# Performance work log

Hardware: AMD Instinct MI355X
Metric: run time of the kernel (lower is better)

The kernel has to match this reference:

```python
import jax, jax.numpy as jnp
import numpy as np

B, S, F = 4, 2048, 1024
D_K = 1024


def setup_inputs() -> dict:
    key = jax.random.key(0)
    ks = jax.random.split(key, 9)
    s_in = 1.0 / np.sqrt(F)
    s_dk = 1.0 / np.sqrt(D_K)
    return {
        "x": jax.random.normal(ks[0], (B, S, F), jnp.float32),
        "Wq": jax.random.normal(ks[1], (F, D_K), jnp.float32) * s_in,
        "bq": jax.random.normal(ks[2], (D_K,), jnp.float32) * s_in,
        "Wk": jax.random.normal(ks[3], (F, D_K), jnp.float32) * s_in,
        "bk": jax.random.normal(ks[4], (D_K,), jnp.float32) * s_in,
        "Wv": jax.random.normal(ks[5], (F, D_K), jnp.float32) * s_in,
        "bv": jax.random.normal(ks[6], (D_K,), jnp.float32) * s_in,
        "Wo": jax.random.normal(ks[7], (D_K, F), jnp.float32) * s_dk,
        "bo": jax.random.normal(ks[8], (F,), jnp.float32) * s_dk,
    }


def reference(x, Wq, bq, Wk, bk, Wv, bv, Wo, bo):
    d_k = Wq.shape[1]
    # init_keys(x): keys/values are projections of the same sequence
    keys = jnp.einsum("bsf,fd->bsd", x, Wk) + bk      # [B,S,d_k]
    values = jnp.einsum("bsf,fd->bsd", x, Wv) + bv    # [B,S,d_k]
    queries = jnp.einsum("bsf,fd->bsd", x, Wq) + bq   # [B,S,d_k]
    # scores[b, q, k] = <queries[b,q], keys[b,k]> / sqrt(d_k)
    scores = jnp.einsum("bqd,bkd->bqk", queries, keys) / jnp.sqrt(
        jnp.asarray(d_k, x.dtype)
    )
    # NOTE: original softmaxes over dim=-2, i.e. over the QUERY axis
    attn = jax.nn.softmax(scores, axis=-2)            # [B,Sq,Sk]
    ctx = jnp.einsum("bqk,bkd->bqd", attn, values)    # [B,S,d_k]
    out = jnp.einsum("bqd,df->bqf", ctx, Wo) + bo     # [B,S,F]
    return out
```

## Files before the change

kernel.cpp:

```cpp
#include <hip/hip_runtime.h>
#include <hip/hip_bf16.h>
#include <cstdint>

typedef __bf16 bf16_t;
typedef __bf16 bf16x8 __attribute__((ext_vector_type(8)));
typedef float  floatx4 __attribute__((ext_vector_type(4)));

typedef const __attribute__((address_space(1))) unsigned int* gptr_t;
typedef __attribute__((address_space(3))) unsigned int* lptr_t;

static __device__ __forceinline__ void gl2lds16(const bf16_t* g, bf16_t* l) {
  __builtin_amdgcn_global_load_lds((gptr_t)g, (lptr_t)l, 16, 0, 0);
}

template<int OUT_BF16, int HAS_BIAS, int EXP_COLSUM, int SPLIT3>
__global__ __launch_bounds__(256, 4)
void gemm_nt(const bf16_t* __restrict__ A, const bf16_t* __restrict__ Bt,
             void* __restrict__ Cv, const float* __restrict__ bias,
             float* __restrict__ L,
             int M, int N, int K, int ldC, float alpha,
             long sA, long sB, long sC,
             long co0, long co1, long co2)
{
  __shared__ __align__(16) bf16_t smem[2 * 128 * 32];
  bf16_t* As = smem;
  bf16_t* Bs = smem + 128 * 32;

  const int bz = blockIdx.z;
  A  += bz * sA;
  Bt += bz * sB;

  const int gn0 = blockIdx.x * 128;
  const int m0  = blockIdx.y * 128;
  const int tid  = threadIdx.x;
  const int lane = tid & 63;
  const int wave = tid >> 6;
  const int wm   = (wave >> 1) * 64;
  const int wn   = (wave & 1) * 64;
  const int lm   = lane & 15;
  const int quad = lane >> 4;

  int n0 = gn0;
  bf16_t* Cb = (bf16_t*)Cv;
  float*  Cf = (float*)Cv;
  if (SPLIT3) {
    const int which = gn0 >> 10;
    n0 = gn0 & 1023;
    Cb += (which == 0) ? co0 : (which == 1) ? co1 : co2;
  }

  const int srow   = lane >> 2;
  const int schunk = (lane & 3) * 8;

  floatx4 acc[4][4];
#pragma unroll
  for (int i = 0; i < 4; ++i)
#pragma unroll
    for (int j = 0; j < 4; ++j)
      acc[i][j] = (floatx4)(0.f);

  for (int kk = 0; kk < K; kk += 32) {
    __syncthreads();
#pragma unroll
    for (int t = 0; t < 2; ++t) {
      const int r = wave * 32 + t * 16 + srow;
      gl2lds16(A  + (long)(m0  + r) * K + kk + schunk, &As[r * 32 + schunk]);
      gl2lds16(Bt + (long)(gn0 + r) * K + kk + schunk, &Bs[r * 32 + schunk]);
    }
    __syncthreads();

    bf16x8 af[4], bfr[4];
#pragma unroll
    for (int i = 0; i < 4; ++i)
      af[i] = *(const bf16x8*)&As[(wm + i * 16 + lm) * 32 + quad * 8];
#pragma unroll
    for (int j = 0; j < 4; ++j)
      bfr[j] = *(const bf16x8*)&Bs[(wn + j * 16 + lm) * 32 + quad * 8];
#pragma unroll
    for (int i = 0; i < 4; ++i)
#pragma unroll
      for (int j = 0; j < 4; ++j)
        acc[i][j] = __builtin_amdgcn_mfma_f32_16x16x32_bf16(af[i], bfr[j],
                                                            acc[i][j], 0, 0, 0);
  }

  if (OUT_BF16) {
    __syncthreads();
    bf16_t* myEp = smem + wave * (16 * 68);
    const int r8 = lane >> 3;
    const int c8 = lane & 7;
    float cs[4] = {0.f, 0.f, 0.f, 0.f};
#pragma unroll
    for (int i = 0; i < 4; ++i) {
#pragma unroll
      for (int j = 0; j < 4; ++j) {
        const float bv = HAS_BIAS ? bias[gn0 + wn + j * 16 + lm] : 0.f;
#pragma unroll
        for (int r = 0; r < 4; ++r) {
          float v = alpha * acc[i][j][r];
          if (EXP_COLSUM) { v = __expf(v); cs[j] += v; }
          v += bv;
          myEp[(quad * 4 + r) * 68 + j * 16 + lm] = (bf16_t)v;
        }
      }
#pragma unroll
      for (int t = 0; t < 2; ++t) {
        const int row = t * 8 + r8;
        const bf16x8 vv = *(const bf16x8*)&myEp[row * 68 + c8 * 8];
        *(bf16x8*)&Cb[bz * sC + (long)(m0 + wm + i * 16 + row) * ldC
                      + n0 + wn + c8 * 8] = vv;
      }
    }
    if (EXP_COLSUM) {
#pragma unroll
      for (int j = 0; j < 4; ++j) {
        float v = cs[j];
        v += __shfl_xor(v, 16);
        v += __shfl_xor(v, 32);
        if (quad == 0)
          atomicAdd(&L[bz * N + gn0 + wn + j * 16 + lm], v);
      }
    }
  } else {
#pragma unroll
    for (int j = 0; j < 4; ++j) {
      const int cn = n0 + wn + j * 16 + lm;
      const float bv = HAS_BIAS ? bias[gn0 + wn + j * 16 + lm] : 0.f;
#pragma unroll
      for (int i = 0; i < 4; ++i) {
        const int rbase = m0 + wm + i * 16 + quad * 4;
#pragma unroll
        for (int r = 0; r < 4; ++r)
          Cf[bz * sC + (long)(rbase + r) * ldC + cn] = alpha * acc[i][j][r] + bv;
      }
    }
  }
}

template<typename TIN>
__global__ void transpose_to_bf16(const TIN* __restrict__ in, bf16_t* __restrict__ out,
                                  int rows, int cols, long sIn, long sOut)
{
  __shared__ float tile[32][33];
  const int bz = blockIdx.z;
  in  += bz * sIn;
  out += bz * sOut;
  const int c0 = blockIdx.x * 32;
  const int r0 = blockIdx.y * 32;
  const int tx = threadIdx.x;
  const int ty = threadIdx.y;
#pragma unroll
  for (int i = 0; i < 32; i += 8)
    tile[ty + i][tx] = (float)in[(long)(r0 + ty + i) * cols + (c0 + tx)];
  __syncthreads();
#pragma unroll
  for (int i = 0; i < 32; i += 8)
    out[(long)(c0 + ty + i) * rows + (r0 + tx)] = (bf16_t)tile[tx][ty + i];
}

__global__ void transpose3_to_bf16(const float* __restrict__ w0,
                                   const float* __restrict__ w1,
                                   const float* __restrict__ w2,
                                   bf16_t* __restrict__ out, int rows, int cols)
{
  __shared__ float tile[32][33];
  const int z = blockIdx.z;
  const float* in = (z == 0) ? w0 : (z == 1) ? w1 : w2;
  out += (long)z * rows * cols;
  const int c0 = blockIdx.x * 32;
  const int r0 = blockIdx.y * 32;
  const int tx = threadIdx.x;
  const int ty = threadIdx.y;
#pragma unroll
  for (int i = 0; i < 32; i += 8)
    tile[ty + i][tx] = in[(long)(r0 + ty + i) * cols + (c0 + tx)];
  __syncthreads();
#pragma unroll
  for (int i = 0; i < 32; i += 8)
    out[(long)(c0 + ty + i) * rows + (r0 + tx)] = (bf16_t)tile[tx][ty + i];
}

__global__ void cvt_f32_to_bf16(const float* __restrict__ in, bf16_t* __restrict__ out,
                                long n)
{
  const long i = ((long)blockIdx.x * blockDim.x + threadIdx.x) * 4;
  if (i >= n) return;
  const float4 v = *(const float4*)(in + i);
  struct alignas(8) B4 { bf16_t a, b, c, d; };
  B4 o; o.a = (bf16_t)v.x; o.b = (bf16_t)v.y; o.c = (bf16_t)v.z; o.d = (bf16_t)v.w;
  *(B4*)(out + i) = o;
}

__global__ void concat3(const float* __restrict__ a, const float* __restrict__ b,
                        const float* __restrict__ c, float* __restrict__ o)
{
  const int i = blockIdx.x * blockDim.x + threadIdx.x;
  const float* s = (i < 1024) ? a : (i < 2048) ? b : c;
  o[i] = s[i & 1023];
}

__global__ __launch_bounds__(256)
void scale_vt(bf16_t* __restrict__ Vt, const float* __restrict__ L, int S)
{
  const long base = ((long)blockIdx.x * blockDim.x + threadIdx.x) * 8;
  const int b  = (int)(base >> 21);
  const int s0 = (int)(base & (long)(S - 1));
  const float* Lb = L + b * S + s0;
  bf16x8 v = *(const bf16x8*)(Vt + base);
#pragma unroll
  for (int j = 0; j < 8; ++j)
    v[j] = (bf16_t)((float)v[j] / Lb[j]);
  *(bf16x8*)(Vt + base) = v;
}

extern "C" void kernel_launch(void* const* d_in, const int* in_sizes, int n_in,
                              void* d_out, int out_size, void* d_ws, size_t ws_size,
                              hipStream_t stream)
{
  const int Bz = 4, S = 2048, F = 1024, DK = 1024;
  const int M = Bz * S;

  const float* x  = (const float*)d_in[0];
  const float* Wq = (const float*)d_in[1];
  const float* bq = (const float*)d_in[2];
  const float* Wk = (const float*)d_in[3];
  const float* bk = (const float*)d_in[4];
  const float* Wv = (const float*)d_in[5];
  const float* bv = (const float*)d_in[6];
  const float* Wo = (const float*)d_in[7];
  const float* bo = (const float*)d_in[8];

  char* ws = (char*)d_ws;
  const size_t MB = 1ull << 20;
  bf16_t* Xb   = (bf16_t*)(ws + 0);
  bf16_t* V    = (bf16_t*)(ws + 16 * MB);
  bf16_t* Sc   = (bf16_t*)(ws + 0);
  bf16_t* Q    = (bf16_t*)(ws + 32 * MB);
  bf16_t* Ctx  = (bf16_t*)(ws + 32 * MB);
  bf16_t* Kb   = (bf16_t*)(ws + 48 * MB);
  bf16_t* Vt   = (bf16_t*)(ws + 64 * MB);
  float*  bcat = (float*)(ws + 64 * MB);
  bf16_t* WcatT= (bf16_t*)(ws + 80 * MB);
  float*  L    = (float*)(ws + 80 * MB);
  bf16_t* WoT  = (bf16_t*)(ws + 86 * MB);

  const long coQ = 16 * MB;
  const long coK = 24 * MB;
  const long coV =  8 * MB;

  cvt_f32_to_bf16<<<(M * F) / 1024, 256, 0, stream>>>(x, Xb, (long)M * F);

  dim3 tb(32, 8);
  transpose3_to_bf16<<<dim3(DK / 32, F / 32, 3), tb, 0, stream>>>(Wq, Wk, Wv, WcatT, F, DK);
  transpose_to_bf16<float><<<dim3(F / 32, DK / 32, 1), tb, 0, stream>>>(Wo, WoT, DK, F, 0, 0);
  concat3<<<12, 256, 0, stream>>>(bq, bk, bv, bcat);

  gemm_nt<1, 1, 0, 1><<<dim3(3 * DK / 128, M / 128, 1), 256, 0, stream>>>(
      Xb, WcatT, (void*)ws, bcat, nullptr, M, 3 * DK, F, DK, 1.f,
      0, 0, 0, coQ, coK, coV);

  transpose_to_bf16<bf16_t><<<dim3(DK / 32, S / 32, Bz), tb, 0, stream>>>(
      V, Vt, S, DK, (long)S * DK, (long)S * DK);

  hipMemsetAsync(L, 0, (size_t)Bz * S * sizeof(float), stream);
  gemm_nt<1, 0, 1, 0><<<dim3(S / 128, S / 128, Bz), 256, 0, stream>>>(
      Q, Kb, Sc, nullptr, L, S, S, DK, S, 0.03125f,
      (long)S * DK, (long)S * DK, (long)S * S, 0, 0, 0);

  scale_vt<<<((long)Bz * DK * S / 8) / 256, 256, 0, stream>>>(Vt, L, S);

  gemm_nt<1, 0, 0, 0><<<dim3(DK / 128, S / 128, Bz), 256, 0, stream>>>(
      Sc, Vt, Ctx, nullptr, nullptr, S, DK, S, DK, 1.f,
      (long)S * S, (long)S * DK, (long)S * DK, 0, 0, 0);

  gemm_nt<0, 1, 0, 0><<<dim3(F / 128, M / 128, 1), 256, 0, stream>>>(
      Ctx, WoT, d_out, bo, nullptr, M, F, DK, F, 1.f,
      0, 0, 0, 0, 0, 0);
}
```

Measured before the change: 319.0 us.

## Fuse V transpose into QKV GEMM epilogue, merge weight transposes, remap tiles per XCD

The QKV projection GEMM's epilogue now writes the V slice directly in transposed [B, D, S] layout through shared memory. This removes the separate bf16 transpose kernel and the round trip of V through global memory. The Wq/Wk/Wv/Wo transposes are merged into one launch, and the bias concat kernel is dropped by passing the three bias pointers directly. Each GEMM also remaps block IDs in groups of 8 so that consecutive tiles land on the same XCD for better L2 locality. The price is a different store pattern for the V tiles: short strided 16-byte column writes.

New measurement: 307.5 us. 3.6% less time.

```diff
diff --git a/kernel.cpp b/kernel.cpp
--- a/kernel.cpp
+++ b/kernel.cpp
@@ -16,11 +16,14 @@
 template<int OUT_BF16, int HAS_BIAS, int EXP_COLSUM, int SPLIT3>
 __global__ __launch_bounds__(256, 4)
 void gemm_nt(const bf16_t* __restrict__ A, const bf16_t* __restrict__ Bt,
-             void* __restrict__ Cv, const float* __restrict__ bias,
+             void* __restrict__ Cv,
+             const float* __restrict__ b0, const float* __restrict__ b1,
+             const float* __restrict__ b2,
              float* __restrict__ L,
              int M, int N, int K, int ldC, float alpha,
              long sA, long sB, long sC,
-             long co0, long co1, long co2)
+             long co0, long co1, long co2,
+             int mbShift, int ldTv, long sTv)
 {
   __shared__ __align__(16) bf16_t smem[2 * 128 * 32];
   bf16_t* As = smem;
@@ -30,8 +33,20 @@
   A  += bz * sA;
   Bt += bz * sB;
 
-  const int gn0 = blockIdx.x * 128;
-  const int m0  = blockIdx.y * 128;
+  int bx = blockIdx.x, by = blockIdx.y;
+  {
+    const int gx = gridDim.x;
+    const int nb = gx * gridDim.y;
+    if ((nb & 7) == 0) {
+      const int id = bx + gx * by;
+      const int T  = (id & 7) * (nb >> 3) + (id >> 3);
+      bx = T % gx;
+      by = T / gx;
+    }
+  }
+
+  const int gn0 = bx * 128;
+  const int m0  = by * 128;
   const int tid  = threadIdx.x;
   const int lane = tid & 63;
   const int wave = tid >> 6;
@@ -41,12 +56,15 @@
   const int quad = lane >> 4;
 
   int n0 = gn0;
+  int which = 0;
   bf16_t* Cb = (bf16_t*)Cv;
   float*  Cf = (float*)Cv;
+  const float* bias = b0;
   if (SPLIT3) {
-    const int which = gn0 >> 10;
+    which = gn0 >> 10;
     n0 = gn0 & 1023;
     Cb += (which == 0) ? co0 : (which == 1) ? co1 : co2;
+    bias = (which == 0) ? b0 : (which == 1) ? b1 : b2;
   }
 
   const int srow   = lane >> 2;
@@ -84,7 +102,30 @@
                                                             acc[i][j], 0, 0, 0);
   }
 
-  if (OUT_BF16) {
+  if (SPLIT3 && which == 2) {
+    __syncthreads();
+    bf16_t* myT = smem + wave * (16 * 68);
+    const int b  = m0 >> mbShift;
+    const int s0 = m0 & ((1 << mbShift) - 1);
+    const int r8 = lane >> 3;
+    const int c8 = lane & 7;
+#pragma unroll
+    for (int j = 0; j < 4; ++j) {
+      const float bv = HAS_BIAS ? bias[n0 + wn + j * 16 + lm] : 0.f;
+#pragma unroll
+      for (int i = 0; i < 4; ++i)
+#pragma unroll
+        for (int r = 0; r < 4; ++r)
+          myT[lm * 68 + i * 16 + quad * 4 + r] = (bf16_t)(acc[i][j][r] + bv);
+#pragma unroll
+      for (int t = 0; t < 2; ++t) {
+        const int nr = t * 8 + r8;
+        const bf16x8 vv = *(const bf16x8*)&myT[nr * 68 + c8 * 8];
+        *(bf16x8*)&Cb[(long)b * sTv + (long)(n0 + wn + j * 16 + nr) * ldTv
+                      + s0 + wm + c8 * 8] = vv;
+      }
+    }
+  } else if (OUT_BF16) {
     __syncthreads();
     bf16_t* myEp = smem + wave * (16 * 68);
     const int r8 = lane >> 3;
@@ -94,7 +135,7 @@
     for (int i = 0; i < 4; ++i) {
 #pragma unroll
       for (int j = 0; j < 4; ++j) {
-        const float bv = HAS_BIAS ? bias[gn0 + wn + j * 16 + lm] : 0.f;
+        const float bv = HAS_BIAS ? bias[n0 + wn + j * 16 + lm] : 0.f;
 #pragma unroll
         for (int r = 0; r < 4; ++r) {
           float v = alpha * acc[i][j][r];
@@ -125,7 +166,7 @@
 #pragma unroll
     for (int j = 0; j < 4; ++j) {
       const int cn = n0 + wn + j * 16 + lm;
-      const float bv = HAS_BIAS ? bias[gn0 + wn + j * 16 + lm] : 0.f;
+      const float bv = HAS_BIAS ? bias[n0 + wn + j * 16 + lm] : 0.f;
 #pragma unroll
       for (int i = 0; i < 4; ++i) {
         const int rbase = m0 + wm + i * 16 + quad * 4;
@@ -137,47 +178,28 @@
   }
 }
 
-template<typename TIN>
-__global__ void transpose_to_bf16(const TIN* __restrict__ in, bf16_t* __restrict__ out,
-                                  int rows, int cols, long sIn, long sOut)
+__global__ void transpose4_to_bf16(const float* __restrict__ w0,
+                                   const float* __restrict__ w1,
+                                   const float* __restrict__ w2,
+                                   const float* __restrict__ w3,
+                                   bf16_t* __restrict__ outQKV,
+                                   bf16_t* __restrict__ outO)
 {
   __shared__ float tile[32][33];
-  const int bz = blockIdx.z;
-  in  += bz * sIn;
-  out += bz * sOut;
+  const int z = blockIdx.z;
+  const float* in = (z == 0) ? w0 : (z == 1) ? w1 : (z == 2) ? w2 : w3;
+  bf16_t* out = (z < 3) ? outQKV + (long)z * 1024 * 1024 : outO;
   const int c0 = blockIdx.x * 32;
   const int r0 = blockIdx.y * 32;
   const int tx = threadIdx.x;
   const int ty = threadIdx.y;
 #pragma unroll
   for (int i = 0; i < 32; i += 8)
-    tile[ty + i][tx] = (float)in[(long)(r0 + ty + i) * cols + (c0 + tx)];
+    tile[ty + i][tx] = in[(long)(r0 + ty + i) * 1024 + (c0 + tx)];
   __syncthreads();
 #pragma unroll
   for (int i = 0; i < 32; i += 8)
-    out[(long)(c0 + ty + i) * rows + (r0 + tx)] = (bf16_t)tile[tx][ty + i];
-}
-
-__global__ void transpose3_to_bf16(const float* __restrict__ w0,
-                                   const float* __restrict__ w1,
-                                   const float* __restrict__ w2,
-                                   bf16_t* __restrict__ out, int rows, int cols)
-{
-  __shared__ float tile[32][33];
-  const int z = blockIdx.z;
-  const float* in = (z == 0) ? w0 : (z == 1) ? w1 : w2;
-  out += (long)z * rows * cols;
-  const int c0 = blockIdx.x * 32;
-  const int r0 = blockIdx.y * 32;
-  const int tx = threadIdx.x;
-  const int ty = threadIdx.y;
-#pragma unroll
-  for (int i = 0; i < 32; i += 8)
-    tile[ty + i][tx] = in[(long)(r0 + ty + i) * cols + (c0 + tx)];
-  __syncthreads();
-#pragma unroll
-  for (int i = 0; i < 32; i += 8)
-    out[(long)(c0 + ty + i) * rows + (r0 + tx)] = (bf16_t)tile[tx][ty + i];
+    out[(long)(c0 + ty + i) * 1024 + (r0 + tx)] = (bf16_t)tile[tx][ty + i];
 }
 
 __global__ void cvt_f32_to_bf16(const float* __restrict__ in, bf16_t* __restrict__ out,
@@ -189,14 +211,6 @@
   struct alignas(8) B4 { bf16_t a, b, c, d; };
   B4 o; o.a = (bf16_t)v.x; o.b = (bf16_t)v.y; o.c = (bf16_t)v.z; o.d = (bf16_t)v.w;
   *(B4*)(out + i) = o;
-}
-
-__global__ void concat3(const float* __restrict__ a, const float* __restrict__ b,
-                        const float* __restrict__ c, float* __restrict__ o)
-{
-  const int i = blockIdx.x * blockDim.x + threadIdx.x;
-  const float* s = (i < 1024) ? a : (i < 2048) ? b : c;
-  o[i] = s[i & 1023];
 }
 
 __global__ __launch_bounds__(256)
@@ -233,47 +247,40 @@
   char* ws = (char*)d_ws;
   const size_t MB = 1ull << 20;
   bf16_t* Xb   = (bf16_t*)(ws + 0);
-  bf16_t* V    = (bf16_t*)(ws + 16 * MB);
   bf16_t* Sc   = (bf16_t*)(ws + 0);
   bf16_t* Q    = (bf16_t*)(ws + 32 * MB);
   bf16_t* Ctx  = (bf16_t*)(ws + 32 * MB);
   bf16_t* Kb   = (bf16_t*)(ws + 48 * MB);
   bf16_t* Vt   = (bf16_t*)(ws + 64 * MB);
-  float*  bcat = (float*)(ws + 64 * MB);
   bf16_t* WcatT= (bf16_t*)(ws + 80 * MB);
   float*  L    = (float*)(ws + 80 * MB);
   bf16_t* WoT  = (bf16_t*)(ws + 86 * MB);
 
   const long coQ = 16 * MB;
   const long coK = 24 * MB;
-  const long coV =  8 * MB;
+  const long coV = 32 * MB;
 
   cvt_f32_to_bf16<<<(M * F) / 1024, 256, 0, stream>>>(x, Xb, (long)M * F);
 
-  dim3 tb(32, 8);
-  transpose3_to_bf16<<<dim3(DK / 32, F / 32, 3), tb, 0, stream>>>(Wq, Wk, Wv, WcatT, F, DK);
-  transpose_to_bf16<float><<<dim3(F / 32, DK / 32, 1), tb, 0, stream>>>(Wo, WoT, DK, F, 0, 0);
-  concat3<<<12, 256, 0, stream>>>(bq, bk, bv, bcat);
+  transpose4_to_bf16<<<dim3(32, 32, 4), dim3(32, 8), 0, stream>>>(
+      Wq, Wk, Wv, Wo, WcatT, WoT);
 
   gemm_nt<1, 1, 0, 1><<<dim3(3 * DK / 128, M / 128, 1), 256, 0, stream>>>(
-      Xb, WcatT, (void*)ws, bcat, nullptr, M, 3 * DK, F, DK, 1.f,
-      0, 0, 0, coQ, coK, coV);
-
-  transpose_to_bf16<bf16_t><<<dim3(DK / 32, S / 32, Bz), tb, 0, stream>>>(
-      V, Vt, S, DK, (long)S * DK, (long)S * DK);
+      Xb, WcatT, (void*)ws, bq, bk, bv, nullptr, M, 3 * DK, F, DK, 1.f,
+      0, 0, 0, coQ, coK, coV, 11, S, (long)DK * S);
 
   hipMemsetAsync(L, 0, (size_t)Bz * S * sizeof(float), stream);
   gemm_nt<1, 0, 1, 0><<<dim3(S / 128, S / 128, Bz), 256, 0, stream>>>(
-      Q, Kb, Sc, nullptr, L, S, S, DK, S, 0.03125f,
-      (long)S * DK, (long)S * DK, (long)S * S, 0, 0, 0);
+      Q, Kb, Sc, nullptr, nullptr, nullptr, L, S, S, DK, S, 0.03125f,
+      (long)S * DK, (long)S * DK, (long)S * S, 0, 0, 0, 0, 0, 0);
 
   scale_vt<<<((long)Bz * DK * S / 8) / 256, 256, 0, stream>>>(Vt, L, S);
 
   gemm_nt<1, 0, 0, 0><<<dim3(DK / 128, S / 128, Bz), 256, 0, stream>>>(
-      Sc, Vt, Ctx, nullptr, nullptr, S, DK, S, DK, 1.f,
-      (long)S * S, (long)S * DK, (long)S * DK, 0, 0, 0);
+      Sc, Vt, Ctx, nullptr, nullptr, nullptr, nullptr, S, DK, S, DK, 1.f,
+      (long)S * S, (long)S * DK, (long)S * DK, 0, 0, 0, 0, 0, 0);
 
   gemm_nt<0, 1, 0, 0><<<dim3(F / 128, M / 128, 1), 256, 0, stream>>>(
-      Ctx, WoT, d_out, bo, nullptr, M, F, DK, F, 1.f,
-      0, 0, 0, 0, 0, 0);
-}
+      Ctx, WoT, d_out, bo, nullptr, nullptr, nullptr, M, F, DK, F, 1.f,
+      0, 0, 0, 0, 0, 0, 0, 0, 0);
+}
```
